# Kernel tuning notes

Hardware: AMD Instinct MI355X
Metric: run time of the kernel (lower is better)

The kernel has to match this reference:

```python
import jax, jax.numpy as jnp
import numpy as np

N, E, B, IN = 20000, 320000, 64, 192


def setup_inputs() -> dict:
    key = jax.random.key(0)
    ks = iter(jax.random.split(key, 80))
    d = {}
    d["x"] = jax.random.normal(next(ks), (N, IN), jnp.float32)
    d["edge_index"] = jax.random.randint(next(ks), (2, E), 0, N - 1)  # +1 shift stays < N
    d["edge_attr"] = jax.random.normal(next(ks), (E,), jnp.float32)
    d["batch"] = jnp.sort(jax.random.randint(next(ks), (N,), 0, B))

    def lin(i, o):
        w = jax.random.normal(next(ks), (i, o), jnp.float32) * (1.0 / i ** 0.5)
        return w, jnp.zeros((o,), jnp.float32)

    dims = [(IN, 4, 64), (256, 4, 64), (256, 6, 32)]  # (in_ch, heads, out_ch) per conv
    for l, (ic, h, c) in enumerate(dims, 1):
        hc = h * c
        d[f"Wq{l}"], d[f"bq{l}"] = lin(ic, hc)
        d[f"Wk{l}"], d[f"bk{l}"] = lin(ic, hc)
        d[f"Wv{l}"], d[f"bv{l}"] = lin(ic, hc)
        d[f"We{l}"] = jax.random.normal(next(ks), (1, hc), jnp.float32)  # lin_edge, no bias
        d[f"Ws{l}"], d[f"bs{l}"] = lin(ic, hc)  # root/skip weight
    d["g1"] = jnp.ones((256,), jnp.float32); d["be1"] = jnp.zeros((256,), jnp.float32)
    d["g2"] = jnp.ones((256,), jnp.float32); d["be2"] = jnp.zeros((256,), jnp.float32)
    d["fc1_w"], d["fc1_b"] = lin(192, 32)
    d["fc2_w"], d["fc2_b"] = lin(32, 2)
    return d


def seg_softmax(s, seg, n):
    # per-destination-node softmax over edges, [E, H]
    m = jax.ops.segment_max(s, seg, num_segments=n)
    m = jnp.where(jnp.isfinite(m), m, 0.0)
    ex = jnp.exp(s - m[seg])
    den = jax.ops.segment_sum(ex, seg, num_segments=n)
    return ex / (den[seg] + 1e-16)


def tconv(x, src, dst, e, Wq, bq, Wk, bk, Wv, bv, We, Ws, bs, h, c):
    # PyG TransformerConv (concat=True, root_weight=True, beta=False, eval -> no dropout)
    n = x.shape[0]
    q = (x @ Wq + bq).reshape(n, h, c)
    k = (x @ Wk + bk).reshape(n, h, c)
    v = (x @ Wv + bv).reshape(n, h, c)
    ee = (e @ We).reshape(-1, h, c)           # [E, h, c] edge embedding
    kj = k[src] + ee                           # gather keys along edges
    scores = jnp.einsum('ehc,ehc->eh', q[dst], kj) * (1.0 / c ** 0.5)
    alpha = seg_softmax(scores, dst, n)        # [E, h]
    msg = (v[src] + ee) * alpha[..., None]
    out = jax.ops.segment_sum(msg, dst, num_segments=n).reshape(n, h * c)
    return out + x @ Ws + bs, alpha


def ln(x, g, b):
    mu = x.mean(-1, keepdims=True)
    var = x.var(-1, keepdims=True)
    return g * (x - mu) / jnp.sqrt(var + 1e-5) + b


def _forward(x, edge_index, edge_attr, batch, Wq1, bq1, Wk1, bk1, Wv1, bv1, We1, Ws1, bs1, Wq2, bq2, Wk2, bk2, Wv2, bv2, We2, Ws2, bs2, Wq3, bq3, Wk3, bk3, Wv3, bv3, We3, Ws3, bs3, g1, be1, g2, be2, fc1_w, fc1_b, fc2_w, fc2_b):
    ei = edge_index + 1                       # replicates `edge_index += 1` in source
    src, dst = ei[0], ei[1]
    e = edge_attr[:, None]                    # edge_dim = 1
    x1, a1 = tconv(x, src, dst, e, Wq1, bq1, Wk1, bk1, Wv1, bv1, We1, Ws1, bs1, 4, 64)
    x1 = jax.nn.relu(ln(x1, g1, be1))
    x2, a2 = tconv(x1, src, dst, e, Wq2, bq2, Wk2, bk2, Wv2, bv2, We2, Ws2, bs2, 4, 64)
    x2 = jax.nn.relu(ln(x2, g2, be2))
    x3, a3 = tconv(x2, src, dst, e, Wq3, bq3, Wk3, bk3, Wv3, bv3, We3, Ws3, bs3, 6, 32)
    x3 = jax.nn.relu(x3)                      # note: norm3 exists in __init__ but is never applied
    xr = x + x3
    cnt = jax.ops.segment_sum(jnp.ones((xr.shape[0],), xr.dtype), batch, num_segments=B)
    pooled = jax.ops.segment_sum(xr, batch, num_segments=B) / jnp.maximum(cnt, 1.0)[:, None]
    h = jax.nn.relu(pooled @ fc1_w + fc1_b)
    logits = h @ fc2_w + fc2_b
    return logits, a1, a2, a3


def reference(x, edge_index, edge_attr, batch, Wq1, bq1, Wk1, bk1, Wv1, bv1, We1, Ws1, bs1, Wq2, bq2, Wk2, bk2, Wv2, bv2, We2, Ws2, bs2, Wq3, bq3, Wk3, bk3, Wv3, bv3, We3, Ws3, bs3, g1, be1, g2, be2, fc1_w, fc1_b, fc2_w, fc2_b):
    return _forward(x, edge_index, edge_attr, batch, Wq1, bq1, Wk1, bk1, Wv1, bv1, We1, Ws1, bs1, Wq2, bq2, Wk2, bk2, Wv2, bv2, We2, Ws2, bs2, Wq3, bq3, Wk3, bk3, Wv3, bv3, We3, Ws3, bs3, g1, be1, g2, be2, fc1_w, fc1_b, fc2_w, fc2_b)
```

## Files before the change

kernel.cpp:

```cpp
#include <hip/hip_runtime.h>
#include <cstdint>
#include <cstddef>

#define DEVINL __device__ __forceinline__

typedef short s16x8 __attribute__((ext_vector_type(8)));
typedef float f32x4 __attribute__((ext_vector_type(4)));
typedef unsigned short u16x4 __attribute__((ext_vector_type(4)));
typedef unsigned short u16x8 __attribute__((ext_vector_type(8)));

DEVINL unsigned short f2bf(float f) {
  unsigned u = __float_as_uint(f);
  unsigned r = (u + 0x7FFFu + ((u >> 16) & 1u)) >> 16;
  return (unsigned short)r;
}
DEVINL float bf2f(unsigned short b) { return __uint_as_float(((unsigned)b) << 16); }

DEVINL void gl16(const unsigned short* g, unsigned short* l) {
  __builtin_amdgcn_global_load_lds(
      (const __attribute__((address_space(1))) unsigned int*)g,
      (__attribute__((address_space(3))) unsigned int*)l, 16, 0, 0);
}

__global__ __launch_bounds__(256) void fill_i32(int* __restrict__ p, int val, int n) {
  int i = blockIdx.x * 256 + threadIdx.x;
  if (i < n) p[i] = val;
}


__global__ __launch_bounds__(256) void cvt_split(const float* __restrict__ in,
                                                 unsigned short* __restrict__ hi,
                                                 unsigned short* __restrict__ lo, int n) {
  int i = blockIdx.x * 256 + threadIdx.x;
  if (i >= n) return;
  float f = in[i];
  unsigned short h = f2bf(f);
  float r = f - bf2f(h);
  hi[i] = h;
  lo[i] = f2bf(r);
}

struct CvtWArgs {
  const float* W[12];
  int K[12];
  int M[12];
};
__global__ __launch_bounds__(256) void cvt_w_all(CvtWArgs a,
                                                 unsigned short* __restrict__ Wh,
                                                 unsigned short* __restrict__ Wl) {
  int tid = blockIdx.x * 256 + threadIdx.x;
  int mat = tid >> 16;
  int off = tid & 65535;
  if (mat >= 12) return;
  int K = a.K[mat], M = a.M[mat];
  if (off >= K * M) return;
  int k = off / M, m = off - k * M;
  float f = a.W[mat][off];
  unsigned short h = f2bf(f);
  float r = f - bf2f(h);
  size_t dst = (size_t)mat * 65536 + (size_t)m * K + k;
  Wh[dst] = h;
  Wl[dst] = f2bf(r);
}

struct GemmArgs {
  const unsigned short* Wh[4];
  const unsigned short* Wl[4];
  const float* bias[4];
  float* out[4];
  int obf[4];
};

template <int KTOT>
__global__ __launch_bounds__(256, 3) void gemm4_lds(
    const unsigned short* __restrict__ Ah, const unsigned short* __restrict__ Al,
    GemmArgs args, int N, int M) {
  const int BK = 64;
  __shared__ unsigned short ash[128 * 64];
  __shared__ unsigned short asl[128 * 64];
  __shared__ unsigned short wsh[64 * 64];
  __shared__ unsigned short wsl[64 * 64];
  int tid = threadIdx.x;
  int wave = tid >> 6, lane = tid & 63;
  int lrow = lane & 15, quad = lane >> 4;
  int mt = M >> 6;
  int ntile = mt * 4;
  int id = blockIdx.x, nwg = gridDim.x;
  int q8 = nwg >> 3, r8 = nwg & 7;
  int xcd = id & 7, j8 = id >> 3;
  int wg = (xcd < r8 ? xcd * (q8 + 1) : r8 * (q8 + 1) + (xcd - r8) * q8) + j8;
  int by = wg / ntile;
  int bxx = wg - by * ntile;
  int z = bxx / mt;
  int colTile = bxx - z * mt;
  int row0 = by * 128;
  int col0 = colTile * 64;
  const unsigned short* __restrict__ Wh = args.Wh[z];
  const unsigned short* __restrict__ Wl = args.Wl[z];
  const bool full = (args.obf[z] == 0);

  int lr8 = lane >> 3;
  int kq = lane & 7;

  f32x4 acc[2][4] = {};

  for (int k0 = 0; k0 < KTOT; k0 += BK) {
    __syncthreads();
#pragma unroll
    for (int i = 0; i < 4; i++) {
      int s = wave + i * 4;
      int row = s * 8 + lr8;
      int gr = row0 + row; if (gr >= N) gr = N - 1;
      size_t gofs = (size_t)gr * KTOT + k0 + ((kq ^ (row & 7)) * 8);
      gl16(Ah + gofs, ash + s * 512);
      gl16(Al + gofs, asl + s * 512);
    }
#pragma unroll
    for (int i = 0; i < 2; i++) {
      int s = wave + i * 4;
      int row = s * 8 + lr8;
      size_t gofs = (size_t)(col0 + row) * KTOT + k0 + ((kq ^ (row & 7)) * 8);
      gl16(Wh + gofs, wsh + s * 512);
      if (full) gl16(Wl + gofs, wsl + s * 512);
    }
    asm volatile("s_waitcnt vmcnt(0)" ::: "memory");
    __syncthreads();
#pragma unroll
    for (int kk = 0; kk < 2; kk++) {
      s16x8 fah[2], fal[2], fbh[4], fbl[4];
#pragma unroll
      for (int rf = 0; rf < 2; rf++) {
        int r = wave * 32 + rf * 16 + lrow;
        int sq = (kk * 4 + quad) ^ (lrow & 7);
        fah[rf] = *(const s16x8*)(ash + r * 64 + sq * 8);
        fal[rf] = *(const s16x8*)(asl + r * 64 + sq * 8);
      }
#pragma unroll
      for (int cf = 0; cf < 4; cf++) {
        int cc = cf * 16 + lrow;
        int sq = (kk * 4 + quad) ^ (lrow & 7);
        fbh[cf] = *(const s16x8*)(wsh + cc * 64 + sq * 8);
        if (full) fbl[cf] = *(const s16x8*)(wsl + cc * 64 + sq * 8);
      }
#pragma unroll
      for (int rf = 0; rf < 2; rf++)
#pragma unroll
        for (int cf = 0; cf < 4; cf++) {
          acc[rf][cf] = __builtin_amdgcn_mfma_f32_16x16x32_bf16(fah[rf], fbh[cf], acc[rf][cf], 0, 0, 0);
          acc[rf][cf] = __builtin_amdgcn_mfma_f32_16x16x32_bf16(fal[rf], fbh[cf], acc[rf][cf], 0, 0, 0);
          if (full)
            acc[rf][cf] = __builtin_amdgcn_mfma_f32_16x16x32_bf16(fah[rf], fbl[cf], acc[rf][cf], 0, 0, 0);
        }
    }
  }
  const float* __restrict__ bias = args.bias[z];
  int obf = args.obf[z];
  if (obf == 0) {
    float* __restrict__ C = args.out[z];
#pragma unroll
    for (int cf = 0; cf < 4; cf++) {
      int col = col0 + cf * 16 + lrow;
      float bv = bias[col];
#pragma unroll
      for (int rf = 0; rf < 2; rf++) {
        int rb = row0 + wave * 32 + rf * 16 + quad * 4;
#pragma unroll
        for (int r = 0; r < 4; r++) {
          int rr = rb + r;
          if (rr < N) C[(size_t)rr * M + col] = acc[rf][cf][r] + bv;
        }
      }
    }
  } else {
    __syncthreads();
#pragma unroll
    for (int cf = 0; cf < 4; cf++) {
      int col = cf * 16 + lrow;
      float bv = bias[col0 + col];
#pragma unroll
      for (int rf = 0; rf < 2; rf++) {
        int rl = wave * 32 + rf * 16 + quad * 4;
#pragma unroll
        for (int r = 0; r < 4; r++)
          ash[(rl + r) * 64 + col] = f2bf(acc[rf][cf][r] + bv);
      }
    }
    __syncthreads();
    unsigned short* __restrict__ C = (unsigned short*)args.out[z];
#pragma unroll
    for (int i = 0; i < 4; i++) {
      int c = tid + i * 256;
      int row = c >> 3, g8 = c & 7;
      int rr = row0 + row;
      if (rr < N)
        *(u16x8*)(C + (size_t)rr * M + col0 + g8 * 8) =
            *(const u16x8*)(ash + row * 64 + g8 * 8);
    }
  }
}


__global__ __launch_bounds__(256) void hist_dst(const int* __restrict__ dst,
                                                int* __restrict__ cnt, int E) {
  int e = blockIdx.x * 256 + threadIdx.x;
  if (e < E) atomicAdd(&cnt[dst[e] + 1], 1);
}

__global__ __launch_bounds__(1024) void scan_hist(const int* __restrict__ cnt,
                                                  int* __restrict__ start,
                                                  int* __restrict__ off, int N) {
  __shared__ int sums[1024];
  const int CH = 20;
  int t = threadIdx.x;
  int base = t * CH;
  int local[CH];
  int tot = 0;
  if (base < N) {
#pragma unroll
    for (int i = 0; i < CH; i++) { local[i] = cnt[base + i]; tot += local[i]; }
  }
  sums[t] = tot;
  __syncthreads();
  for (int d = 1; d < 1024; d <<= 1) {
    int v = (t >= d) ? sums[t - d] : 0;
    __syncthreads();
    sums[t] += v;
    __syncthreads();
  }
  if (base < N) {
    int run = (t == 0) ? 0 : sums[t - 1];
#pragma unroll
    for (int i = 0; i < CH; i++) { start[base + i] = run; off[base + i] = run; run += local[i]; }
    if (base + CH == N) start[N] = run;
  }
}

__global__ __launch_bounds__(256) void scatter_edges(
    const int* __restrict__ src, const int* __restrict__ dst,
    const float* __restrict__ ea, int* __restrict__ off,
    int2* __restrict__ se, int* __restrict__ eid_s, int E) {
  int e = blockIdx.x * 256 + threadIdx.x;
  if (e >= E) return;
  int d = dst[e] + 1;
  int pos = atomicAdd(&off[d], 1);
  se[pos] = make_int2(src[e] + 1, __float_as_int(ea[e]));
  eid_s[pos] = e;
}

template <int H, int ACT, int MODE>
__global__ __launch_bounds__(256) void attn_fused(
    const unsigned short* __restrict__ q, const unsigned short* __restrict__ kb,
    const unsigned short* __restrict__ vb, const float* __restrict__ We,
    const int* __restrict__ start, const int2* __restrict__ se,
    const int* __restrict__ eid_s,
    float* __restrict__ sc, float* __restrict__ outp,
    float* __restrict__ alpha, int Nn, float scale,
    const float* __restrict__ gam, const float* __restrict__ bet,
    unsigned short* __restrict__ hi, unsigned short* __restrict__ lo) {
  const int HC = ACT * 8;
  const int LPH2 = ACT / H;
  const int D = 6;
  int w = (blockIdx.x * 256 + threadIdx.x) >> 6;
  int lane = threadIdx.x & 63;
  if (w >= Nn) return;
  int b = start[w], e = start[w + 1];
  int hlane = lane & 31, half = lane >> 5;
  bool act = hlane < ACT;
  int idx = hlane * 8;
  int head = hlane / LPH2;
  float q8[8], We8[8];
#pragma unroll
  for (int j = 0; j < 8; j++) { q8[j] = 0.f; We8[j] = 0.f; }
  if (act) {
    u16x8 qv = *(const u16x8*)(q + (size_t)w * HC + idx);
#pragma unroll
    for (int j = 0; j < 8; j++) q8[j] = bf2f(qv[j]);
    float4 w0 = *(const float4*)(We + idx);
    float4 w1 = *(const float4*)(We + idx + 4);
    We8[0] = w0.x; We8[1] = w0.y; We8[2] = w0.z; We8[3] = w0.w;
    We8[4] = w1.x; We8[5] = w1.y; We8[6] = w1.z; We8[7] = w1.w;
  }
  float qwe = 0.f;
#pragma unroll
  for (int j = 0; j < 8; j++) qwe = fmaf(q8[j], We8[j], qwe);
#pragma unroll
  for (int mm = 1; mm < LPH2; mm <<= 1) qwe += __shfl_xor(qwe, mm, 64);

  float l = 0.f, tv = 0.f;
  float accv[8] = {0.f, 0.f, 0.f, 0.f, 0.f, 0.f, 0.f, 0.f};

  auto step = [&](u16x8 kc, u16x8 vc, float eav, int pairpos) {
    bool vld = (pairpos + half) < e;
    float p = 0.f;
#pragma unroll
    for (int j = 0; j < 8; j++) p = fmaf(q8[j], bf2f(kc[j]), p);
#pragma unroll
    for (int mm = 1; mm < LPH2; mm <<= 1) p += __shfl_xor(p, mm, 64);
    float es = __expf((p + eav * qwe) * scale);
    if (!vld) es = 0.f;
    if (act && vld && (hlane % LPH2) == 0)
      sc[(size_t)(pairpos + half) * H + head] = es;
    l += es;
    tv = fmaf(es, eav, tv);
#pragma unroll
    for (int j = 0; j < 8; j++) accv[j] = fmaf(es, bf2f(vc[j]), accv[j]);
  };

  u16x8 z8 = {0, 0, 0, 0, 0, 0, 0, 0};
  u16x8 kS[D], vS[D];
  float eaS[D];
#pragma unroll
  for (int j = 0; j < D; j++) { kS[j] = z8; vS[j] = z8; eaS[j] = 0.f; }

  auto preload = [&](int pairpos, int st) {
    int pp = pairpos + half;
    int pc = pp < e ? pp : (e - 1);
    int2 pr = se[pc];
    int s = pr.x;
    eaS[st] = __int_as_float(pr.y);
    if (act) {
      kS[st] = *(const u16x8*)(kb + (size_t)s * HC + idx);
      vS[st] = *(const u16x8*)(vb + (size_t)s * HC + idx);
    }
  };

#pragma unroll
  for (int j = 0; j < D; j++) if (b + 2 * j < e) preload(b + 2 * j, j);

  for (int pos = b; pos < e; pos += 2 * D) {
#pragma unroll
    for (int j = 0; j < D; j++) {
      int pp = pos + 2 * j;
      if (pp < e) {
        u16x8 kc = kS[j];
        u16x8 vc = vS[j];
        float ec = eaS[j];
        if (pp + 2 * D < e) preload(pp + 2 * D, j);
        step(kc, vc, ec, pp);
      }
    }
  }

  l += __shfl_xor(l, 32, 64);
  tv += __shfl_xor(tv, 32, 64);
#pragma unroll
  for (int j = 0; j < 8; j++) accv[j] += __shfl_xor(accv[j], 32, 64);

  float invl = 1.0f / (l + 1e-16f);
  if (MODE == 1) {
    if (half == 0) {
      const float* orow = outp + (size_t)w * HC + idx;
      float4 o0 = *(const float4*)orow;
      float4 o1 = *(const float4*)(orow + 4);
      float y[8] = {o0.x, o0.y, o0.z, o0.w, o1.x, o1.y, o1.z, o1.w};
#pragma unroll
      for (int j = 0; j < 8; j++) y[j] += (accv[j] + tv * We8[j]) * invl;
      float s = 0.f, s2 = 0.f;
#pragma unroll
      for (int j = 0; j < 8; j++) { s += y[j]; s2 = fmaf(y[j], y[j], s2); }
#pragma unroll
      for (int mm = 1; mm < 32; mm <<= 1) {
        s += __shfl_xor(s, mm, 64);
        s2 += __shfl_xor(s2, mm, 64);
      }
      float mu = s * (1.0f / 256.0f);
      float var = s2 * (1.0f / 256.0f) - mu * mu;
      float rinv = rsqrtf(var + 1e-5f);
      float4 g0 = *(const float4*)(gam + idx);
      float4 g1v = *(const float4*)(gam + idx + 4);
      float4 b0 = *(const float4*)(bet + idx);
      float4 b1 = *(const float4*)(bet + idx + 4);
      float gg[8] = {g0.x, g0.y, g0.z, g0.w, g1v.x, g1v.y, g1v.z, g1v.w};
      float bb[8] = {b0.x, b0.y, b0.z, b0.w, b1.x, b1.y, b1.z, b1.w};
      u16x8 yh, yl;
#pragma unroll
      for (int j = 0; j < 8; j++) {
        float t = fmaxf(fmaf((y[j] - mu) * rinv, gg[j], bb[j]), 0.f);
        unsigned short hh = f2bf(t);
        yh[j] = hh;
        yl[j] = f2bf(t - bf2f(hh));
      }
      *(u16x8*)(hi + (size_t)w * HC + idx) = yh;
      *(u16x8*)(lo + (size_t)w * HC + idx) = yl;
    }
  } else {
    if (act && half == 0) {
      float* orow = outp + (size_t)w * HC + idx;
      float4 o0 = *(float4*)orow;
      float4 o1 = *(float4*)(orow + 4);
      o0.x += (accv[0] + tv * We8[0]) * invl;
      o0.y += (accv[1] + tv * We8[1]) * invl;
      o0.z += (accv[2] + tv * We8[2]) * invl;
      o0.w += (accv[3] + tv * We8[3]) * invl;
      o1.x += (accv[4] + tv * We8[4]) * invl;
      o1.y += (accv[5] + tv * We8[5]) * invl;
      o1.z += (accv[6] + tv * We8[6]) * invl;
      o1.w += (accv[7] + tv * We8[7]) * invl;
      *(float4*)orow = o0;
      *(float4*)(orow + 4) = o1;
    }
  }
  {
    int len = e - b;
    const int PCH = 64 / H;
    int p_of = lane / H;
    int h_of = lane - p_of * H;
    float myinv = __shfl(invl, h_of * LPH2, 64);
    __threadfence_block();
    for (int base = 0; base < len; base += PCH) {
      int po = base + p_of;
      if (p_of < PCH && po < len) {
        int pos = b + po;
        float es = sc[(size_t)pos * H + h_of];
        alpha[(size_t)eid_s[pos] * H + h_of] = es * myinv;
      }
    }
  }
}


__global__ __launch_bounds__(192) void resid_pool2(
    const float* __restrict__ x, const float* __restrict__ x3,
    const int* __restrict__ batch, float* __restrict__ pooled,
    float* __restrict__ cnt, int N, int R) {
  int col = threadIdx.x;
  int r0 = blockIdx.x * R;
  int r1 = min(r0 + R, N);
  if (r0 >= N) return;
  float acc = 0.f;
  int cur = batch[r0];
  int run = 0;
  for (int r = r0; r < r1; r++) {
    int b = batch[r];
    if (b != cur) {
      atomicAdd(&pooled[cur * 192 + col], acc);
      if (col == 0) atomicAdd(&cnt[cur], (float)run);
      acc = 0.f; run = 0; cur = b;
    }
    size_t i = (size_t)r * 192 + col;
    acc += x[i] + fmaxf(x3[i], 0.f);
    run++;
  }
  atomicAdd(&pooled[cur * 192 + col], acc);
  if (col == 0) atomicAdd(&cnt[cur], (float)run);
}

__global__ __launch_bounds__(64) void head_mlp(
    const float* __restrict__ pooled, const float* __restrict__ cnt,
    const float* __restrict__ fc1w, const float* __restrict__ fc1b,
    const float* __restrict__ fc2w, const float* __restrict__ fc2b,
    float* __restrict__ logits) {
  int b = blockIdx.x;
  int t = threadIdx.x;
  __shared__ float p[192];
  __shared__ float hbuf[32];
  float inv = 1.0f / fmaxf(cnt[b], 1.0f);
  for (int i = t; i < 192; i += 64) p[i] = pooled[b * 192 + i] * inv;
  __syncthreads();
  if (t < 32) {
    float acc = fc1b[t];
    for (int i = 0; i < 192; i++) acc = fmaf(p[i], fc1w[i * 32 + t], acc);
    hbuf[t] = fmaxf(acc, 0.f);
  }
  __syncthreads();
  if (t < 2) {
    float acc = fc2b[t];
    for (int j = 0; j < 32; j++) acc = fmaf(hbuf[j], fc2w[j * 2 + t], acc);
    logits[b * 2 + t] = acc;
  }
}

static inline int divup(int a, int b) { return (a + b - 1) / b; }

extern "C" void kernel_launch(void* const* d_in, const int* in_sizes, int n_in,
                              void* d_out, int out_size, void* d_ws, size_t ws_size,
                              hipStream_t stream) {
  const int N = 20000, E = 320000, B = 64;
  const float* x     = (const float*)d_in[0];
  const int*   ei    = (const int*)d_in[1];
  const float* eattr = (const float*)d_in[2];
  const int*   batch = (const int*)d_in[3];
  const int* srcp = ei;
  const int* dstp = ei + E;

  const float* Wq[3]; const float* bq[3]; const float* Wk[3]; const float* bk[3];
  const float* Wv[3]; const float* bv[3]; const float* We[3]; const float* Ws[3];
  const float* bs[3];
  for (int l = 0; l < 3; l++) {
    int base = 4 + l * 9;
    Wq[l] = (const float*)d_in[base + 0]; bq[l] = (const float*)d_in[base + 1];
    Wk[l] = (const float*)d_in[base + 2]; bk[l] = (const float*)d_in[base + 3];
    Wv[l] = (const float*)d_in[base + 4]; bv[l] = (const float*)d_in[base + 5];
    We[l] = (const float*)d_in[base + 6];
    Ws[l] = (const float*)d_in[base + 7]; bs[l] = (const float*)d_in[base + 8];
  }
  const float* g1  = (const float*)d_in[31]; const float* be1 = (const float*)d_in[32];
  const float* g2  = (const float*)d_in[33]; const float* be2 = (const float*)d_in[34];
  const float* fc1w = (const float*)d_in[35]; const float* fc1b = (const float*)d_in[36];
  const float* fc2w = (const float*)d_in[37]; const float* fc2b = (const float*)d_in[38];

  float* out = (float*)d_out;
  float* logits = out;
  float* a1 = out + 128;
  float* a2 = a1 + (size_t)E * 4;
  float* a3 = a2 + (size_t)E * 4;

  float* ws = (float*)d_ws;
  size_t o = 0;
  float* qb = ws + o; o += (size_t)N * 256;
  float* kvb = ws + o; o += (size_t)N * 256;
  float* xa = ws + o; o += (size_t)N * 256;
  float* xb = ws + o; o += (size_t)N * 256;
  float* sc = ws + o; o += (size_t)E * 6;
  int*   cntb  = (int*)(ws + o); o += N;
  int*   startb= (int*)(ws + o); o += N + 1;
  int*   offb  = (int*)(ws + o); o += N + 1;
  int2*  se    = (int2*)(ws + o); o += (size_t)E * 2;
  int*   eid_s = (int*)(ws + o); o += E;
  float* pooled = ws + o; o += (size_t)B * 192;
  float* cnt    = ws + o; o += B;
  unsigned short* Ah = (unsigned short*)(ws + o); o += (size_t)N * 128;
  unsigned short* Al = (unsigned short*)(ws + o); o += (size_t)N * 128;
  unsigned short* Wh12 = (unsigned short*)(ws + o); o += (size_t)12 * 32768;
  unsigned short* Wl12 = (unsigned short*)(ws + o); o += (size_t)12 * 32768;

  unsigned short* qh = (unsigned short*)qb;
  unsigned short* kh = (unsigned short*)kvb;
  unsigned short* vh = kh + (size_t)N * 256;

  dim3 blk(256);

  struct LayerCfg { int K, M; float scale; };
  LayerCfg cfg[3] = {
    {192, 256, 0.125f},
    {256, 256, 0.125f},
    {256, 192, 0.1767766952966369f},
  };
  CvtWArgs cwa;
  for (int l = 0; l < 3; l++) {
    cwa.W[l * 4 + 0] = Wq[l]; cwa.W[l * 4 + 1] = Wk[l];
    cwa.W[l * 4 + 2] = Wv[l]; cwa.W[l * 4 + 3] = Ws[l];
    for (int zz = 0; zz < 4; zz++) {
      cwa.K[l * 4 + zz] = cfg[l].K; cwa.M[l * 4 + zz] = cfg[l].M;
    }
  }
  cvt_w_all<<<12 * 65536 / 256, blk, 0, stream>>>(cwa, Wh12, Wl12);

  fill_i32<<<divup(N, 256), blk, 0, stream>>>(cntb, 0, N);
  hist_dst<<<divup(E, 256), blk, 0, stream>>>(dstp, cntb, E);
  scan_hist<<<1, dim3(1024), 0, stream>>>(cntb, startb, offb, N);
  scatter_edges<<<divup(E, 256), blk, 0, stream>>>(srcp, dstp, eattr, offb,
                                                  se, eid_s, E);

  float*       lay_out[3] = {xb, xb, xa};
  float*       alpha_out[3] = {a1, a2, a3};
  const float* gams[3] = {g1, g2, nullptr};
  const float* bets[3] = {be1, be2, nullptr};

  cvt_split<<<divup(N * 192, 256), blk, 0, stream>>>(x, Ah, Al, N * 192);

  int stripes = divup(N, 128);
  for (int l = 0; l < 3; l++) {
    int M = cfg[l].M;
    GemmArgs ga;
    float* outs[4] = {(float*)qh, (float*)kh, (float*)vh, lay_out[l]};
    const float* biases[4] = {bq[l], bk[l], bv[l], bs[l]};
    int obfs[4] = {1, 1, 1, 0};
    for (int z = 0; z < 4; z++) {
      ga.Wh[z] = Wh12 + (size_t)(l * 4 + z) * 65536;
      ga.Wl[z] = Wl12 + (size_t)(l * 4 + z) * 65536;
      ga.bias[z] = biases[z];
      ga.out[z] = outs[z];
      ga.obf[z] = obfs[z];
    }
    dim3 gg((M >> 6) * 4 * stripes);
    if (l == 0)      gemm4_lds<192><<<gg, blk, 0, stream>>>(Ah, Al, ga, N, M);
    else             gemm4_lds<256><<<gg, blk, 0, stream>>>(Ah, Al, ga, N, M);

    dim3 gat(divup(N * 64, 256));
    if (l < 2) {
      attn_fused<4, 32, 1><<<gat, blk, 0, stream>>>(
          qh, kh, vh, We[l], startb, se, eid_s, sc, lay_out[l],
          alpha_out[l], N, cfg[l].scale, gams[l], bets[l], Ah, Al);
    } else {
      attn_fused<6, 24, 0><<<gat, blk, 0, stream>>>(
          qh, kh, vh, We[l], startb, se, eid_s, sc, lay_out[l],
          alpha_out[l], N, cfg[l].scale, nullptr, nullptr, nullptr, nullptr);
    }
  }

  fill_i32<<<divup(B * 192 + B, 256), blk, 0, stream>>>((int*)pooled, 0, B * 192 + B);
  resid_pool2<<<divup(N, 32), dim3(192), 0, stream>>>(x, xa, batch, pooled, cnt, N, 32);
  head_mlp<<<B, dim3(64), 0, stream>>>(pooled, cnt, fc1w, fc1b, fc2w, fc2b, logits);
}
```

Before: 541.6 us.

## Merge setup conversion and zero-fill kernels into one prologue; lower attention D

Replaces four separate launches (weight conversion, x hi/lo split, count zeroing, pooled zeroing) with a single prologue kernel that picks its work by block index. This removes launch and inter-kernel gaps. It also lowers the attention kernel's constant D from 6 to 4, which changes that kernel's edge batching or unrolling depth. The pooled buffer is now zeroed before the layers run rather than just before pooling. This is safe as long as nothing writes to that buffer in between.

```diff
diff --git a/kernel.cpp b/kernel.cpp
--- a/kernel.cpp
+++ b/kernel.cpp
@@ -25,19 +25,6 @@
 __global__ __launch_bounds__(256) void fill_i32(int* __restrict__ p, int val, int n) {
   int i = blockIdx.x * 256 + threadIdx.x;
   if (i < n) p[i] = val;
-}
-
-
-__global__ __launch_bounds__(256) void cvt_split(const float* __restrict__ in,
-                                                 unsigned short* __restrict__ hi,
-                                                 unsigned short* __restrict__ lo, int n) {
-  int i = blockIdx.x * 256 + threadIdx.x;
-  if (i >= n) return;
-  float f = in[i];
-  unsigned short h = f2bf(f);
-  float r = f - bf2f(h);
-  hi[i] = h;
-  lo[i] = f2bf(r);
 }
 
 struct CvtWArgs {
@@ -45,22 +32,42 @@
   int K[12];
   int M[12];
 };
-__global__ __launch_bounds__(256) void cvt_w_all(CvtWArgs a,
-                                                 unsigned short* __restrict__ Wh,
-                                                 unsigned short* __restrict__ Wl) {
-  int tid = blockIdx.x * 256 + threadIdx.x;
-  int mat = tid >> 16;
-  int off = tid & 65535;
-  if (mat >= 12) return;
-  int K = a.K[mat], M = a.M[mat];
-  if (off >= K * M) return;
-  int k = off / M, m = off - k * M;
-  float f = a.W[mat][off];
-  unsigned short h = f2bf(f);
-  float r = f - bf2f(h);
-  size_t dst = (size_t)mat * 65536 + (size_t)m * K + k;
-  Wh[dst] = h;
-  Wl[dst] = f2bf(r);
+
+__global__ __launch_bounds__(256) void prologue(
+    CvtWArgs a, unsigned short* __restrict__ Wh, unsigned short* __restrict__ Wl,
+    const float* __restrict__ xin, unsigned short* __restrict__ Ah,
+    unsigned short* __restrict__ Al, int nsplit,
+    int* __restrict__ cntb, int ncnt, int* __restrict__ poolz, int npool) {
+  int bid = blockIdx.x;
+  if (bid < 3072) {
+    int tid = bid * 256 + threadIdx.x;
+    int mat = tid >> 16;
+    int off = tid & 65535;
+    if (mat >= 12) return;
+    int K = a.K[mat], M = a.M[mat];
+    if (off >= K * M) return;
+    int k = off / M, m = off - k * M;
+    float f = a.W[mat][off];
+    unsigned short h = f2bf(f);
+    float r = f - bf2f(h);
+    size_t dst = (size_t)mat * 65536 + (size_t)m * K + k;
+    Wh[dst] = h;
+    Wl[dst] = f2bf(r);
+  } else if (bid < 3072 + 79) {
+    int i = (bid - 3072) * 256 + threadIdx.x;
+    if (i < ncnt) cntb[i] = 0;
+  } else if (bid < 3200) {
+    int i = (bid - 3151) * 256 + threadIdx.x;
+    if (i < npool) poolz[i] = 0;
+  } else {
+    int i = (bid - 3200) * 256 + threadIdx.x;
+    if (i >= nsplit) return;
+    float f = xin[i];
+    unsigned short h = f2bf(f);
+    float r = f - bf2f(h);
+    Ah[i] = h;
+    Al[i] = f2bf(r);
+  }
 }
 
 struct GemmArgs {
@@ -259,7 +266,7 @@
     unsigned short* __restrict__ hi, unsigned short* __restrict__ lo) {
   const int HC = ACT * 8;
   const int LPH2 = ACT / H;
-  const int D = 6;
+  const int D = 4;
   int w = (blockIdx.x * 256 + threadIdx.x) >> 6;
   int lane = threadIdx.x & 63;
   if (w >= Nn) return;
@@ -544,9 +551,10 @@
       cwa.K[l * 4 + zz] = cfg[l].K; cwa.M[l * 4 + zz] = cfg[l].M;
     }
   }
-  cvt_w_all<<<12 * 65536 / 256, blk, 0, stream>>>(cwa, Wh12, Wl12);
-
-  fill_i32<<<divup(N, 256), blk, 0, stream>>>(cntb, 0, N);
+
+  prologue<<<3200 + divup(N * 192, 256), blk, 0, stream>>>(
+      cwa, Wh12, Wl12, x, Ah, Al, N * 192, cntb, N, (int*)pooled, B * 192 + B);
+
   hist_dst<<<divup(E, 256), blk, 0, stream>>>(dstp, cntb, E);
   scan_hist<<<1, dim3(1024), 0, stream>>>(cntb, startb, offb, N);
   scatter_edges<<<divup(E, 256), blk, 0, stream>>>(srcp, dstp, eattr, offb,
@@ -556,8 +564,6 @@
   float*       alpha_out[3] = {a1, a2, a3};
   const float* gams[3] = {g1, g2, nullptr};
   const float* bets[3] = {be1, be2, nullptr};
-
-  cvt_split<<<divup(N * 192, 256), blk, 0, stream>>>(x, Ah, Al, N * 192);
 
   int stripes = divup(N, 128);
   for (int l = 0; l < 3; l++) {
@@ -589,7 +595,6 @@
     }
   }
 
-  fill_i32<<<divup(B * 192 + B, 256), blk, 0, stream>>>((int*)pooled, 0, B * 192 + B);
   resid_pool2<<<divup(N, 32), dim3(192), 0, stream>>>(x, xa, batch, pooled, cnt, N, 32);
   head_mlp<<<B, dim3(64), 0, stream>>>(pooled, cnt, fc1w, fc1b, fc2w, fc2b, logits);
 }
```

Measured after the change: 529.5 us (median of 2 runs). 2.2% less time.
